# Optimization experiments

Measured on AMD Instinct MI355X. Metric: run time of the kernel, lower is better.

Reference implementation:

```python
import jax, jax.numpy as jnp
import numpy as np

N, E, P, FE = 100000, 400000, 10000, 20000
EMB, L = 300, 5
EPS_BN = 1e-5
EPS_NORM = 1e-12


def setup_inputs() -> dict:
    key = jax.random.key(0)
    ks = iter(jax.random.split(key, 40))

    def nrm(shape, s=0.1):
        return jax.random.normal(next(ks), shape, dtype=jnp.float32) * s

    return {
        "x": jax.random.randint(next(ks), (N, 2), 0, 3),
        "edge_index": jax.random.randint(next(ks), (2, E), 0, N),
        "edge_attr": jax.random.randint(next(ks), (E, 2), 0, 3),
        "frag_batch": jnp.sort(jax.random.randint(next(ks), (N,), 0, P)),
        "frag_edge_index": jax.random.randint(next(ks), (2, FE), 0, P),
        "dangling_edge_attr": jax.random.randint(next(ks), (FE, 2), 0, 3),
        "num_frags": P,
        "atom_emb1": nrm((120, EMB)),
        "atom_emb2": nrm((3, EMB)),
        "gin_e1": nrm((L, 6, EMB)),
        "gin_e2": nrm((L, 3, EMB)),
        "gin_w1": nrm((L, EMB, 2 * EMB), 0.05),
        "gin_b1": jnp.zeros((L, 2 * EMB), jnp.float32),
        "gin_w2": nrm((L, 2 * EMB, EMB), 0.05),
        "gin_b2": jnp.zeros((L, EMB), jnp.float32),
        "bn_g": jnp.ones((L, EMB), jnp.float32),
        "bn_b": jnp.zeros((L, EMB), jnp.float32),
        "proj_w1": nrm((EMB, EMB), 0.05),
        "proj_b1": jnp.zeros((EMB,), jnp.float32),
        "proj_w2": nrm((EMB, EMB), 0.05),
        "proj_b2": jnp.zeros((EMB,), jnp.float32),
        "gcn_w": nrm((EMB, EMB), 0.05),
        "gcn_b": jnp.zeros((EMB,), jnp.float32),
        "gcn_e1": nrm((6, EMB)),
        "gcn_e2": nrm((3, EMB)),
        "cls_w": nrm((EMB, 1), 0.05),
        "cls_b": jnp.zeros((1,), jnp.float32),
    }


def reference(x, edge_index, edge_attr, frag_batch, frag_edge_index,
              dangling_edge_attr, num_frags,
              atom_emb1, atom_emb2, gin_e1, gin_e2, gin_w1, gin_b1, gin_w2,
              gin_b2, bn_g, bn_b, proj_w1, proj_b1, proj_w2, proj_b2,
              gcn_w, gcn_b, gcn_e1, gcn_e2, cls_w, cls_b):
    src, dst = edge_index[0], edge_index[1]
    # --- GNN encoder: 5 GIN layers with edge embeddings + self loops + BN ---
    h = atom_emb1[x[:, 0]] + atom_emb2[x[:, 1]]  # [N, EMB]
    for l in range(L):
        eemb = gin_e1[l][edge_attr[:, 0]] + gin_e2[l][edge_attr[:, 1]]  # [E, EMB]
        agg = jnp.zeros_like(h).at[dst].add(h[src] + eemb)
        # self loops carry bond type 4, direction 0 (pretrain-gnns convention)
        agg = agg + h + (gin_e1[l][4] + gin_e2[l][0])
        h2 = jax.nn.relu(agg @ gin_w1[l] + gin_b1[l]) @ gin_w2[l] + gin_b2[l]
        mu = h2.mean(0)
        var = ((h2 - mu) ** 2).mean(0)  # biased var, torch BN training mode
        h2 = (h2 - mu) * jax.lax.rsqrt(var + EPS_BN) * bn_g[l] + bn_b[l]
        h = h2 if l == L - 1 else jax.nn.relu(h2)
    # --- global mean pool over fragments ---
    seg = jax.ops.segment_sum(h, frag_batch, num_segments=num_frags)
    cnt = jax.ops.segment_sum(jnp.ones((h.shape[0],), h.dtype), frag_batch,
                              num_segments=num_frags)
    pooled = seg / jnp.maximum(cnt, 1.0)[:, None]  # [P, EMB]
    # --- projector MLP ---
    out = jax.nn.relu(pooled @ proj_w1 + proj_b1) @ proj_w2 + proj_b2
    f0 = out / jnp.maximum(jnp.linalg.norm(out, axis=1, keepdims=True), EPS_NORM)
    # --- GCN predictor on symmetrized fragment graph (no self loops) ---
    u = jnp.concatenate([frag_edge_index[0], frag_edge_index[1]])
    v = jnp.concatenate([frag_edge_index[1], frag_edge_index[0]])
    ea = jnp.concatenate([dangling_edge_attr, dangling_edge_attr], axis=0)
    xw = out @ gcn_w + gcn_b
    eemb = gcn_e1[ea[:, 0]] + gcn_e2[ea[:, 1]]
    deg = jnp.zeros((num_frags,), xw.dtype).at[u].add(1.0)
    dis = jnp.where(deg > 0, jax.lax.rsqrt(jnp.maximum(deg, 1.0)), 0.0)
    norm = dis[u] * dis[v]  # deg^-1/2 symmetric normalization
    pred = jnp.zeros_like(xw).at[v].add(norm[:, None] * (xw[u] + eemb))
    f1 = pred / jnp.maximum(jnp.linalg.norm(pred, axis=1, keepdims=True), EPS_NORM)
    f2 = jnp.roll(f1, 1, axis=0)
    # --- classifier on elementwise-max features ---
    pos = jnp.maximum(f0, f1) @ cls_w + cls_b
    neg = jnp.maximum(f0, f2) @ cls_w + cls_b
    return jnp.concatenate([pos, neg], axis=0)[:, 0]  # [2*P]
```

## Files before the change

### kernel.cpp

```cpp
#include <hip/hip_runtime.h>
#include <cstdint>
#include <cstddef>

#define EMB 300
#define EMB2 600
#define NLAYER 5
#define SLD 304
#define KP1 320
#define NP1 640
#define NP2 384
#define SCAN_B 256

typedef short bf16x8 __attribute__((ext_vector_type(8)));
typedef float f32x4 __attribute__((ext_vector_type(4)));
typedef unsigned int u32x4 __attribute__((ext_vector_type(4)));
typedef unsigned short ushort_t;
typedef unsigned int uint_t;

static inline int cdiv(int a, int b) { return (a + b - 1) / b; }

__device__ inline ushort_t f2bf(float v) {
    unsigned u = __float_as_uint(v);
    u += 0x7fffu + ((u >> 16) & 1u);
    return (ushort_t)(u >> 16);
}
__device__ inline float bf2f(ushort_t h) { return __uint_as_float(((unsigned)h) << 16); }

__device__ inline uint_t packbf(float v) {
    ushort_t h = f2bf(v);
    ushort_t l = f2bf(v - bf2f(h));
    return (uint_t)h | ((uint_t)l << 16);
}
__device__ inline u32x4 pack4(f32x4 v) {
    u32x4 w;
    #pragma unroll
    for (int j = 0; j < 4; ++j) w[j] = packbf(v[j]);
    return w;
}

__device__ inline f32x4 bnrelu4(f32x4 v, f32x4 s, f32x4 h, bool use_bn) {
    if (!use_bn) return v;
    f32x4 r;
    #pragma unroll
    for (int j = 0; j < 4; ++j) r[j] = fmaxf(fmaf(v[j], s[j], h[j]), 0.f);
    return r;
}

__global__ __launch_bounds__(256) void zero_kernel(float* __restrict__ p, size_t n)
{
    size_t i = (size_t)blockIdx.x * blockDim.x + threadIdx.x;
    size_t stride = (size_t)gridDim.x * blockDim.x;
    for (; i < n; i += stride) p[i] = 0.f;
}
static inline void launch_zero(float* p, size_t n, hipStream_t s)
{
    int g = (int)((n + 255) / 256);
    if (g > 2048) g = 2048;
    zero_kernel<<<g, 256, 0, s>>>(p, n);
}
__global__ __launch_bounds__(256) void izero_kernel(int* __restrict__ p, int n)
{
    int i = blockIdx.x * 256 + threadIdx.x;
    if (i < n) p[i] = 0;
}

__global__ __launch_bounds__(256) void embed_kernel(
    const int* __restrict__ x, const float* __restrict__ a1,
    const float* __restrict__ a2, float* __restrict__ h, int N)
{
    int idx = blockIdx.x * blockDim.x + threadIdx.x;
    if (idx >= N * EMB) return;
    int row = idx / EMB, col = idx % EMB;
    h[(size_t)row * SLD + col] = a1[x[2 * row] * EMB + col] + a2[x[2 * row + 1] * EMB + col];
}

__global__ __launch_bounds__(256) void count_kernel(
    const int* __restrict__ dst, int* __restrict__ cnt, int E)
{
    int e = blockIdx.x * 256 + threadIdx.x;
    if (e < E) atomicAdd(&cnt[dst[e]], 1);
}

__global__ __launch_bounds__(SCAN_B) void scan_block_kernel(
    const int* __restrict__ in, int* __restrict__ out, int* __restrict__ bsum, int n)
{
    __shared__ int s[SCAN_B];
    int t = threadIdx.x, i = blockIdx.x * SCAN_B + t;
    int v = (i < n) ? in[i] : 0;
    s[t] = v; __syncthreads();
    for (int o = 1; o < SCAN_B; o <<= 1) {
        int xv = (t >= o) ? s[t - o] : 0;
        __syncthreads();
        s[t] += xv;
        __syncthreads();
    }
    if (i < n) out[i] = s[t] - v;
    if (t == SCAN_B - 1) bsum[blockIdx.x] = s[t];
}

__global__ __launch_bounds__(512) void scan_partials_kernel(
    const int* __restrict__ bsum, int* __restrict__ bbase, int nb)
{
    __shared__ int s[512];
    int t = threadIdx.x;
    int v = (t < nb) ? bsum[t] : 0;
    s[t] = v; __syncthreads();
    for (int o = 1; o < 512; o <<= 1) {
        int xv = (t >= o) ? s[t - o] : 0;
        __syncthreads();
        s[t] += xv;
        __syncthreads();
    }
    if (t < nb) bbase[t] = s[t] - v;
}

__global__ __launch_bounds__(256) void scan_add_kernel(
    int* __restrict__ off, const int* __restrict__ bbase, int n, int total)
{
    int i = blockIdx.x * 256 + threadIdx.x;
    if (i < n) off[i] += bbase[i / SCAN_B];
    if (i == 0) off[n] = total;
}

__global__ __launch_bounds__(256) void fill_kernel(
    const int* __restrict__ dst, const int* __restrict__ off,
    int* __restrict__ cursor, int* __restrict__ eid, int E)
{
    int e = blockIdx.x * 256 + threadIdx.x;
    if (e >= E) return;
    int d = dst[e];
    int p = atomicAdd(&cursor[d], 1);
    eid[off[d] + p] = e;
}

__global__ __launch_bounds__(256) void poff_kernel(
    const int* __restrict__ fb, int* __restrict__ poff, int N, int P)
{
    int i = blockIdx.x * 256 + threadIdx.x;
    if (i >= N) return;
    int b = fb[i];
    if (i == 0) { for (int q = 0; q <= b; ++q) poff[q] = 0; }
    else { int a = fb[i - 1]; for (int q = a + 1; q <= b; ++q) poff[q] = i; }
    if (i == N - 1) { for (int q = b + 1; q <= P; ++q) poff[q] = N; }
}

__global__ __launch_bounds__(256) void e12all_kernel(
    const float* __restrict__ ge1, const float* __restrict__ ge2,
    float* __restrict__ E12all)
{
    int idx = blockIdx.x * 256 + threadIdx.x;
    if (idx >= NLAYER * 18 * EMB) return;
    int l = idx / (18 * EMB);
    int rem = idx - l * 18 * EMB;
    int cmb = rem / EMB, c = rem - cmb * EMB;
    E12all[idx] = ge1[(size_t)l * 6 * EMB + (cmb / 3) * EMB + c]
                + ge2[(size_t)l * 3 * EMB + (cmb % 3) * EMB + c];
}

__global__ __launch_bounds__(256) void bn_finalize_kernel(
    const float* __restrict__ stats, const float* __restrict__ g,
    const float* __restrict__ b, float* __restrict__ scale,
    float* __restrict__ shift, float invN)
{
    int c = blockIdx.x * 256 + threadIdx.x;
    if (c >= EMB) return;
    float mu = stats[c] * invN;
    float var = fmaf(-mu, mu, stats[EMB + c] * invN);
    float s = rsqrtf(var + 1e-5f) * g[c];
    scale[c] = s;
    shift[c] = fmaf(-mu, s, b[c]);
}

__global__ __launch_bounds__(256) void gin_gather_il(
    const float* __restrict__ hin, const float* __restrict__ scale,
    const float* __restrict__ shift, int use_bn,
    const int* __restrict__ off, const int* __restrict__ eid,
    const int* __restrict__ src, const int* __restrict__ ea,
    const float* __restrict__ E12, uint_t* __restrict__ Yil, int N)
{
    int node = (blockIdx.x * blockDim.x + threadIdx.x) >> 6;
    int lane = threadIdx.x & 63;
    if (node >= N) return;
    const bool tl = lane < 11;
    const int c0 = lane * 4, c1 = 256 + lane * 4;
    f32x4 sc0 = {1,1,1,1}, sh0 = {0,0,0,0}, sc1 = {1,1,1,1}, sh1 = {0,0,0,0};
    if (use_bn) {
        sc0 = *(const f32x4*)(scale + c0); sh0 = *(const f32x4*)(shift + c0);
        if (tl) { sc1 = *(const f32x4*)(scale + c1); sh1 = *(const f32x4*)(shift + c1); }
    }
    const float* selfrow = E12 + 12 * EMB;
    f32x4 a0, a1 = {0,0,0,0};
    {
        const float* hr = hin + (size_t)node * SLD;
        a0 = bnrelu4(*(const f32x4*)(hr + c0), sc0, sh0, use_bn) + *(const f32x4*)(selfrow + c0);
        if (tl) a1 = bnrelu4(*(const f32x4*)(hr + c1), sc1, sh1, use_bn) + *(const f32x4*)(selfrow + c1);
    }
    int j0 = off[node], j1 = off[node + 1];
    int s = 0, cmb = 0;
    if (j0 < j1) { int e = eid[j0]; s = src[e]; cmb = ea[2 * e] * 3 + ea[2 * e + 1]; }
    for (int j = j0; j < j1; ++j) {
        int sn = 0, cn = 0;
        if (j + 1 < j1) {
            int en = eid[j + 1];
            sn = src[en];
            cn = ea[2 * en] * 3 + ea[2 * en + 1];
        }
        const float* hs = hin + (size_t)s * SLD;
        const float* er = E12 + (size_t)cmb * EMB;
        a0 += bnrelu4(*(const f32x4*)(hs + c0), sc0, sh0, use_bn) + *(const f32x4*)(er + c0);
        if (tl) a1 += bnrelu4(*(const f32x4*)(hs + c1), sc1, sh1, use_bn) + *(const f32x4*)(er + c1);
        s = sn; cmb = cn;
    }
    uint_t* pw = Yil + (size_t)node * SLD;
    *(u32x4*)(pw + c0) = pack4(a0);
    if (tl) *(u32x4*)(pw + c1) = pack4(a1);
}

__global__ __launch_bounds__(256) void gemm_il(
    const uint_t* __restrict__ Ail, int lda, int Mvalid, int Kvalid,
    const ushort_t* __restrict__ Bhi, const ushort_t* __restrict__ Blo, int ldb,
    const float* __restrict__ bias, int Kpad, int Nvalid,
    float* __restrict__ Cf, int ldcf,
    uint_t* __restrict__ Cil, int ldcs,
    int relu, int out_il, float* __restrict__ stats)
{
    __shared__ ushort_t As[2][128][40];
    __shared__ ushort_t Bs[2][128][40];
    __shared__ float cred[128][2];
    const int tid = threadIdx.x;
    const int lane = tid & 63, wid = tid >> 6;
    const int wr = wid >> 1, wc = wid & 1;
    const int lr = lane & 15, ko = (lane >> 4) * 8;

    int gx = gridDim.x;
    int nwg = gx * gridDim.y;
    int flat = blockIdx.y * gx + blockIdx.x;
    if (nwg >= 8) {
        int q = nwg >> 3, r = nwg & 7, xc = flat & 7, s = flat >> 3;
        flat = (xc < r ? xc * (q + 1) : r * (q + 1) + (xc - r) * q) + s;
    }
    const int row0 = (flat / gx) * 128, col0 = (flat % gx) * 128;

    const int srow = tid >> 1;
    const int sc = (tid & 1) * 16;

    const bool arow_ok = (row0 + srow) < Mvalid;
    const uint_t* pA = Ail + (size_t)(row0 + srow) * lda + sc;
    const ushort_t* pBhi = Bhi + (size_t)(col0 + srow) * ldb + sc;
    const ushort_t* pBlo = Blo + (size_t)(col0 + srow) * ldb + sc;
    const u32x4 z4 = {0u, 0u, 0u, 0u};

    f32x4 acc[4][4] = {};
    u32x4 LA[4];
    bf16x8 rB0, rB1, rB2, rB3;

    #pragma unroll
    for (int q = 0; q < 4; ++q) {
        int kc = sc + q * 4;
        LA[q] = (arow_ok && kc < Kvalid) ? *(const u32x4*)(pA + q * 4) : z4;
    }
    rB0 = *(const bf16x8*)(pBhi);     rB1 = *(const bf16x8*)(pBhi + 8);
    rB2 = *(const bf16x8*)(pBlo);     rB3 = *(const bf16x8*)(pBlo + 8);

    for (int k0 = 0; k0 < Kpad; k0 += 32) {
        uint_t hw[8], lw[8];
        #pragma unroll
        for (int i = 0; i < 8; ++i) {
            uint_t w0 = LA[(2 * i) >> 2][(2 * i) & 3];
            uint_t w1 = LA[(2 * i + 1) >> 2][(2 * i + 1) & 3];
            hw[i] = (w0 & 0xFFFFu) | (w1 << 16);
            lw[i] = (w0 >> 16) | (w1 & 0xFFFF0000u);
        }
        *(u32x4*)&As[0][srow][sc]     = (u32x4){hw[0], hw[1], hw[2], hw[3]};
        *(u32x4*)&As[0][srow][sc + 8] = (u32x4){hw[4], hw[5], hw[6], hw[7]};
        *(u32x4*)&As[1][srow][sc]     = (u32x4){lw[0], lw[1], lw[2], lw[3]};
        *(u32x4*)&As[1][srow][sc + 8] = (u32x4){lw[4], lw[5], lw[6], lw[7]};
        *(bf16x8*)&Bs[0][srow][sc]     = rB0;
        *(bf16x8*)&Bs[0][srow][sc + 8] = rB1;
        *(bf16x8*)&Bs[1][srow][sc]     = rB2;
        *(bf16x8*)&Bs[1][srow][sc + 8] = rB3;
        __syncthreads();
        if (k0 + 32 < Kpad) {
            int kn = k0 + 32;
            #pragma unroll
            for (int q = 0; q < 4; ++q) {
                int kc = kn + sc + q * 4;
                LA[q] = (arow_ok && kc < Kvalid) ? *(const u32x4*)(pA + kn + q * 4) : z4;
            }
            rB0 = *(const bf16x8*)(pBhi + kn);     rB1 = *(const bf16x8*)(pBhi + kn + 8);
            rB2 = *(const bf16x8*)(pBlo + kn);     rB3 = *(const bf16x8*)(pBlo + kn + 8);
        }
        bf16x8 afh[4], afl[4], bfh[4], bfl[4];
        #pragma unroll
        for (int f = 0; f < 4; ++f) {
            int ar = wr * 64 + f * 16 + lr;
            afh[f] = *(const bf16x8*)&As[0][ar][ko];
            afl[f] = *(const bf16x8*)&As[1][ar][ko];
            int bc = wc * 64 + f * 16 + lr;
            bfh[f] = *(const bf16x8*)&Bs[0][bc][ko];
            bfl[f] = *(const bf16x8*)&Bs[1][bc][ko];
        }
        #pragma unroll
        for (int f = 0; f < 4; ++f)
            #pragma unroll
            for (int g = 0; g < 4; ++g) {
                acc[f][g] = __builtin_amdgcn_mfma_f32_16x16x32_bf16(afh[f], bfh[g], acc[f][g], 0, 0, 0);
                acc[f][g] = __builtin_amdgcn_mfma_f32_16x16x32_bf16(afh[f], bfl[g], acc[f][g], 0, 0, 0);
                acc[f][g] = __builtin_amdgcn_mfma_f32_16x16x32_bf16(afl[f], bfh[g], acc[f][g], 0, 0, 0);
            }
        __syncthreads();
    }

    float ts[4] = {0.f, 0.f, 0.f, 0.f}, ts2[4] = {0.f, 0.f, 0.f, 0.f};
    #pragma unroll
    for (int f = 0; f < 4; ++f) {
        int grb = row0 + wr * 64 + f * 16 + (lane >> 4) * 4;
        #pragma unroll
        for (int g = 0; g < 4; ++g) {
            int gc = col0 + wc * 64 + g * 16 + lr;
            float bv = (gc < Nvalid) ? bias[gc] : 0.f;
            #pragma unroll
            for (int j = 0; j < 4; ++j) {
                int gr = grb + j;
                float v = acc[f][g][j] + bv;
                if (relu) v = fmaxf(v, 0.f);
                if (out_il) {
                    float vp = (gc < Nvalid) ? v : 0.f;
                    Cil[(size_t)gr * ldcs + gc] = packbf(vp);
                } else if (gr < Mvalid && gc < Nvalid) {
                    Cf[(size_t)gr * ldcf + gc] = v;
                    if (stats) {
                        ts[g] += v;
                        ts2[g] = fmaf(v, v, ts2[g]);
                    }
                }
            }
        }
    }
    if (stats && !out_il) {
        ((float*)cred)[tid] = 0.f;
        __syncthreads();
        #pragma unroll
        for (int g = 0; g < 4; ++g) {
            int cidx = wc * 64 + g * 16 + lr;
            atomicAdd(&cred[cidx][0], ts[g]);
            atomicAdd(&cred[cidx][1], ts2[g]);
        }
        __syncthreads();
        if (tid < 128) {
            int gc = col0 + tid;
            if (gc < Nvalid) {
                atomicAdd(&stats[gc], cred[tid][0]);
                atomicAdd(&stats[EMB + gc], cred[tid][1]);
            }
        }
    }
}

#define TS 64
#define BKK 16
__global__ __launch_bounds__(256) void gemm_bias_act(
    const float* __restrict__ A, const float* __restrict__ W,
    const float* __restrict__ bias, float* __restrict__ C,
    int M, int K, int Nc, int relu_flag)
{
    __shared__ float Asm[BKK][TS + 4];
    __shared__ float Bsm[BKK][TS + 4];
    const int tid = threadIdx.x;
    const int tx = tid & 15, ty = tid >> 4;
    const int row0 = blockIdx.y * TS, col0 = blockIdx.x * TS;
    const int lka = tid & 15, lra = tid >> 4;
    const int lnb = tid & 63, lkb = tid >> 6;
    float acc[4][4] = {};
    for (int k0 = 0; k0 < K; k0 += BKK) {
        #pragma unroll
        for (int i = 0; i < 4; ++i) {
            int rr = lra + 16 * i;
            int gr = row0 + rr, gk = k0 + lka;
            Asm[lka][rr] = (gr < M && gk < K) ? A[(size_t)gr * K + gk] : 0.f;
        }
        #pragma unroll
        for (int i = 0; i < 4; ++i) {
            int kk = lkb + 4 * i;
            int gk = k0 + kk, gn = col0 + lnb;
            Bsm[kk][lnb] = (gk < K && gn < Nc) ? W[(size_t)gk * Nc + gn] : 0.f;
        }
        __syncthreads();
        #pragma unroll
        for (int kk = 0; kk < BKK; ++kk) {
            float a[4], b[4];
            #pragma unroll
            for (int i = 0; i < 4; ++i) a[i] = Asm[kk][ty * 4 + i];
            #pragma unroll
            for (int j = 0; j < 4; ++j) b[j] = Bsm[kk][tx * 4 + j];
            #pragma unroll
            for (int i = 0; i < 4; ++i)
                #pragma unroll
                for (int j = 0; j < 4; ++j)
                    acc[i][j] = fmaf(a[i], b[j], acc[i][j]);
        }
        __syncthreads();
    }
    #pragma unroll
    for (int i = 0; i < 4; ++i) {
        int gr = row0 + ty * 4 + i;
        if (gr >= M) continue;
        #pragma unroll
        for (int j = 0; j < 4; ++j) {
            int gn = col0 + tx * 4 + j;
            if (gn >= Nc) continue;
            float v = acc[i][j] + bias[gn];
            if (relu_flag) v = fmaxf(v, 0.f);
            C[(size_t)gr * Nc + gn] = v;
        }
    }
}

__global__ __launch_bounds__(256) void wsplit_kernel(
    const float* __restrict__ W, int K, int Nc,
    ushort_t* __restrict__ hi, ushort_t* __restrict__ lo, int Kpad, int Npad)
{
    int idx = blockIdx.x * 256 + threadIdx.x;
    if (idx >= Npad * Kpad) return;
    int n = idx / Kpad, k = idx - n * Kpad;
    float v = (n < Nc && k < K) ? W[(size_t)k * Nc + n] : 0.f;
    ushort_t h = f2bf(v);
    hi[idx] = h;
    lo[idx] = f2bf(v - bf2f(h));
}

__global__ __launch_bounds__(256) void pool_gather_kernel(
    const float* __restrict__ hin, const float* __restrict__ scale,
    const float* __restrict__ shift, const int* __restrict__ poff,
    float* __restrict__ pooled, int P)
{
    int p = (blockIdx.x * blockDim.x + threadIdx.x) >> 6;
    int lane = threadIdx.x & 63;
    if (p >= P) return;
    const bool tl = lane < 11;
    const int c0 = lane * 4, c1 = 256 + lane * 4;
    int r0 = poff[p], r1 = poff[p + 1];
    f32x4 s0 = {0,0,0,0}, s1 = {0,0,0,0};
    for (int r = r0; r < r1; ++r) {
        const float* hr = hin + (size_t)r * SLD;
        s0 += *(const f32x4*)(hr + c0);
        if (tl) s1 += *(const f32x4*)(hr + c1);
    }
    float cntf = (float)(r1 - r0);
    float inv = 1.f / fmaxf(cntf, 1.f);
    f32x4 sc0 = *(const f32x4*)(scale + c0), sh0 = *(const f32x4*)(shift + c0);
    f32x4 o0;
    #pragma unroll
    for (int j = 0; j < 4; ++j) o0[j] = fmaf(s0[j], sc0[j], cntf * sh0[j]) * inv;
    float* pr = pooled + (size_t)p * EMB;
    *(f32x4*)(pr + c0) = o0;
    if (tl) {
        f32x4 sc1 = *(const f32x4*)(scale + c1), sh1 = *(const f32x4*)(shift + c1);
        f32x4 o1;
        #pragma unroll
        for (int j = 0; j < 4; ++j) o1[j] = fmaf(s1[j], sc1[j], cntf * sh1[j]) * inv;
        *(f32x4*)(pr + c1) = o1;
    }
}

__global__ __launch_bounds__(256) void normalize_rows_kernel(
    const float* __restrict__ X, float* __restrict__ Y, int M)
{
    int wv = (blockIdx.x * blockDim.x + threadIdx.x) >> 6;
    int lane = threadIdx.x & 63;
    if (wv >= M) return;
    const float* x = X + (size_t)wv * EMB;
    float ss = 0.f;
    for (int c = lane; c < EMB; c += 64) { float v = x[c]; ss = fmaf(v, v, ss); }
    #pragma unroll
    for (int o = 32; o > 0; o >>= 1) ss += __shfl_xor(ss, o, 64);
    float inv = 1.f / fmaxf(sqrtf(ss), 1e-12f);
    float* y = Y + (size_t)wv * EMB;
    for (int c = lane; c < EMB; c += 64) y[c] = x[c] * inv;
}

__global__ __launch_bounds__(256) void deg_kernel(
    const int* __restrict__ fei, float* __restrict__ deg, int FE)
{
    int i = blockIdx.x * blockDim.x + threadIdx.x;
    if (i < 2 * FE) atomicAdd(&deg[fei[i]], 1.f);
}

__global__ __launch_bounds__(256) void gcn_scatter_kernel(
    const float* __restrict__ xw, const int* __restrict__ fei,
    const int* __restrict__ dea, const float* __restrict__ e1,
    const float* __restrict__ e2, const float* __restrict__ deg,
    float* __restrict__ pred, int FE)
{
    int i = (blockIdx.x * blockDim.x + threadIdx.x) >> 6;
    int lane = threadIdx.x & 63;
    if (i >= 2 * FE) return;
    int u = fei[i];
    int v = (i < FE) ? fei[i + FE] : fei[i - FE];
    int er = (i < FE) ? i : i - FE;
    int a0 = dea[2 * er], a1 = dea[2 * er + 1];
    float du = deg[u], dv = deg[v];
    float su = du > 0.f ? rsqrtf(fmaxf(du, 1.f)) : 0.f;
    float sv = dv > 0.f ? rsqrtf(fmaxf(dv, 1.f)) : 0.f;
    float nr = su * sv;
    const float* xu = xw + (size_t)u * EMB;
    const float* t1 = e1 + (size_t)a0 * EMB;
    const float* t2 = e2 + (size_t)a1 * EMB;
    float* pv = pred + (size_t)v * EMB;
    for (int c = lane; c < EMB; c += 64)
        atomicAdd(&pv[c], nr * (xu[c] + t1[c] + t2[c]));
}

__global__ __launch_bounds__(256) void classifier_kernel(
    const float* __restrict__ f0, const float* __restrict__ f1,
    const float* __restrict__ w, const float* __restrict__ b,
    float* __restrict__ out, int P)
{
    int q = (blockIdx.x * blockDim.x + threadIdx.x) >> 6;
    int lane = threadIdx.x & 63;
    if (q >= 2 * P) return;
    int i = (q < P) ? q : q - P;
    int j = (q < P) ? i : (i == 0 ? P - 1 : i - 1);
    const float* a = f0 + (size_t)i * EMB;
    const float* c = f1 + (size_t)j * EMB;
    float s = 0.f;
    for (int k = lane; k < EMB; k += 64) s = fmaf(fmaxf(a[k], c[k]), w[k], s);
    #pragma unroll
    for (int o = 32; o > 0; o >>= 1) s += __shfl_xor(s, o, 64);
    if (lane == 0) out[q] = s + b[0];
}

extern "C" void kernel_launch(void* const* d_in, const int* in_sizes, int n_in,
                              void* d_out, int out_size, void* d_ws, size_t ws_size,
                              hipStream_t stream)
{
    const int*   x     = (const int*)d_in[0];
    const int*   ei    = (const int*)d_in[1];
    const int*   ea    = (const int*)d_in[2];
    const int*   fb    = (const int*)d_in[3];
    const int*   fei   = (const int*)d_in[4];
    const int*   dea   = (const int*)d_in[5];
    const float* atom1 = (const float*)d_in[7];
    const float* atom2 = (const float*)d_in[8];
    const float* ge1   = (const float*)d_in[9];
    const float* ge2   = (const float*)d_in[10];
    const float* w1    = (const float*)d_in[11];
    const float* b1    = (const float*)d_in[12];
    const float* w2    = (const float*)d_in[13];
    const float* b2    = (const float*)d_in[14];
    const float* bng   = (const float*)d_in[15];
    const float* bnb   = (const float*)d_in[16];
    const float* pw1   = (const float*)d_in[17];
    const float* pb1   = (const float*)d_in[18];
    const float* pw2   = (const float*)d_in[19];
    const float* pb2   = (const float*)d_in[20];
    const float* gw    = (const float*)d_in[21];
    const float* gb    = (const float*)d_in[22];
    const float* gcne1 = (const float*)d_in[23];
    const float* gcne2 = (const float*)d_in[24];
    const float* clw   = (const float*)d_in[25];
    const float* clb   = (const float*)d_in[26];
    (void)n_in; (void)ws_size;

    const int N  = in_sizes[0] / 2;
    const int E  = in_sizes[1] / 2;
    const int FE = in_sizes[4] / 2;
    const int P  = out_size / 2;
    const int Mfull = cdiv(N, 128) * 128;
    float* outF = (float*)d_out;

    char* wp = (char*)d_ws;
    auto carve = [&](size_t bytes) -> char* {
        char* r = wp;
        wp += (bytes + 255) & ~(size_t)255;
        return r;
    };
    const size_t bufElems = (size_t)Mfull * SLD;
    char* bufA = carve(bufElems * 4);
    char* bufB = carve(bufElems * 4);
    float* statsAll = (float*)carve((size_t)NLAYER * 2 * EMB * 4);
    float* scaleAll = (float*)carve((size_t)NLAYER * EMB * 4);
    float* shiftAll = (float*)carve((size_t)NLAYER * EMB * 4);
    float* E12all   = (float*)carve((size_t)NLAYER * 18 * EMB * 4);
    float* deg      = (float*)carve((size_t)P * 4);
    int* poff    = (int*)carve((size_t)(P + 1) * 4);
    int* cnt_i   = (int*)carve((size_t)N * 4);
    int* csr_off = (int*)carve((size_t)(N + 1) * 4);
    int* cursor  = (int*)carve((size_t)N * 4);
    int* csr_eid = (int*)carve((size_t)E * 4);
    int* bsum    = (int*)carve(512 * 4);
    int* bbase   = (int*)carve(512 * 4);
    ushort_t* w1t_hi[NLAYER]; ushort_t* w1t_lo[NLAYER];
    ushort_t* w2t_hi[NLAYER]; ushort_t* w2t_lo[NLAYER];
    for (int l = 0; l < NLAYER; ++l) {
        w1t_hi[l] = (ushort_t*)carve((size_t)NP1 * KP1 * 2);
        w1t_lo[l] = (ushort_t*)carve((size_t)NP1 * KP1 * 2);
        w2t_hi[l] = (ushort_t*)carve((size_t)NP2 * NP1 * 2);
        w2t_lo[l] = (ushort_t*)carve((size_t)NP2 * NP1 * 2);
    }

    int chCap = (int)((bufElems * 4) / ((size_t)NP1 * 4));
    chCap &= ~127;
    int nChunks = cdiv(Mfull, chCap);
    int CH = cdiv(Mfull / 128, nChunks) * 128;

    const int gElemsN = cdiv(N * EMB, 256);
    const int NB = cdiv(N, SCAN_B);

    izero_kernel<<<cdiv(N, 256), 256, 0, stream>>>(cnt_i, N);
    count_kernel<<<cdiv(E, 256), 256, 0, stream>>>(ei + E, cnt_i, E);
    scan_block_kernel<<<NB, SCAN_B, 0, stream>>>(cnt_i, csr_off, bsum, N);
    scan_partials_kernel<<<1, 512, 0, stream>>>(bsum, bbase, NB);
    scan_add_kernel<<<cdiv(N, 256), 256, 0, stream>>>(csr_off, bbase, N, E);
    izero_kernel<<<cdiv(N, 256), 256, 0, stream>>>(cursor, N);
    fill_kernel<<<cdiv(E, 256), 256, 0, stream>>>(ei + E, csr_off, cursor, csr_eid, E);
    poff_kernel<<<cdiv(N, 256), 256, 0, stream>>>(fb, poff, N, P);
    e12all_kernel<<<cdiv(NLAYER * 18 * EMB, 256), 256, 0, stream>>>(ge1, ge2, E12all);
    for (int l = 0; l < NLAYER; ++l) {
        wsplit_kernel<<<cdiv(NP1 * KP1, 256), 256, 0, stream>>>(
            w1 + (size_t)l * EMB * EMB2, EMB, EMB2, w1t_hi[l], w1t_lo[l], KP1, NP1);
        wsplit_kernel<<<cdiv(NP2 * NP1, 256), 256, 0, stream>>>(
            w2 + (size_t)l * EMB2 * EMB, EMB2, EMB, w2t_hi[l], w2t_lo[l], NP1, NP2);
    }
    launch_zero(statsAll, (size_t)NLAYER * 2 * EMB, stream);

    embed_kernel<<<gElemsN, 256, 0, stream>>>(x, atom1, atom2, (float*)bufA, N);

    char* ping = bufA;
    char* pong = bufB;
    for (int l = 0; l < NLAYER; ++l) {
        gin_gather_il<<<cdiv(N, 4), 256, 0, stream>>>(
            (const float*)ping,
            scaleAll + (size_t)(l > 0 ? l - 1 : 0) * EMB,
            shiftAll + (size_t)(l > 0 ? l - 1 : 0) * EMB, (l > 0) ? 1 : 0,
            csr_off, csr_eid, ei, ea, E12all + (size_t)l * 18 * EMB,
            (uint_t*)pong, N);
        uint_t* til = (uint_t*)ping;
        for (int c0 = 0; c0 < N; c0 += CH) {
            int rows = min(CH, N - c0);
            int Mt = cdiv(rows, 128);
            gemm_il<<<dim3(NP1 / 128, Mt), 256, 0, stream>>>(
                (const uint_t*)pong + (size_t)c0 * SLD, SLD, rows, EMB,
                w1t_hi[l], w1t_lo[l], KP1,
                b1 + (size_t)l * EMB2, KP1, EMB2,
                nullptr, 0, til, NP1, 1, 1, nullptr);
            gemm_il<<<dim3(NP2 / 128, Mt), 256, 0, stream>>>(
                til, NP1, rows, NP1,
                w2t_hi[l], w2t_lo[l], NP1,
                b2 + (size_t)l * EMB, NP1, EMB,
                (float*)pong + (size_t)c0 * SLD, SLD, nullptr, 0, 0, 0,
                statsAll + (size_t)l * 2 * EMB);
        }
        bn_finalize_kernel<<<cdiv(EMB, 256), 256, 0, stream>>>(
            statsAll + (size_t)l * 2 * EMB, bng + (size_t)l * EMB, bnb + (size_t)l * EMB,
            scaleAll + (size_t)l * EMB, shiftAll + (size_t)l * EMB, 1.f / (float)N);
        char* tmp = ping; ping = pong; pong = tmp;
    }

    float* Af     = (float*)pong;
    float* pooled = Af + 0 * (size_t)P * EMB;
    float* tmpP   = Af + 1 * (size_t)P * EMB;
    float* outp   = Af + 2 * (size_t)P * EMB;
    float* f0     = Af + 3 * (size_t)P * EMB;
    float* xw     = Af + 4 * (size_t)P * EMB;
    float* pred   = Af + 5 * (size_t)P * EMB;
    float* f1     = Af + 6 * (size_t)P * EMB;

    pool_gather_kernel<<<cdiv(P, 4), 256, 0, stream>>>(
        (const float*)ping, scaleAll + (size_t)(NLAYER - 1) * EMB,
        shiftAll + (size_t)(NLAYER - 1) * EMB, poff, pooled, P);

    {
        dim3 g1(cdiv(EMB, TS), cdiv(P, TS));
        gemm_bias_act<<<g1, 256, 0, stream>>>(pooled, pw1, pb1, tmpP, P, EMB, EMB, 1);
        gemm_bias_act<<<g1, 256, 0, stream>>>(tmpP, pw2, pb2, outp, P, EMB, EMB, 0);
        normalize_rows_kernel<<<cdiv(P, 4), 256, 0, stream>>>(outp, f0, P);
    }

    {
        dim3 g1(cdiv(EMB, TS), cdiv(P, TS));
        gemm_bias_act<<<g1, 256, 0, stream>>>(outp, gw, gb, xw, P, EMB, EMB, 0);
        launch_zero(deg, (size_t)P, stream);
        launch_zero(pred, (size_t)P * EMB, stream);
        deg_kernel<<<cdiv(2 * FE, 256), 256, 0, stream>>>(fei, deg, FE);
        gcn_scatter_kernel<<<cdiv(2 * FE, 4), 256, 0, stream>>>(
            xw, fei, dea, gcne1, gcne2, deg, pred, FE);
        normalize_rows_kernel<<<cdiv(P, 4), 256, 0, stream>>>(pred, f1, P);
    }

    classifier_kernel<<<cdiv(2 * P, 4), 256, 0, stream>>>(f0, f1, clw, clb, outF, P);
}
```

Before: 3.405 ms.

## Route projector and GCN GEMMs through split-bf16 MFMA kernel, nontemporal gather stores

Replaces the scalar FP32 tiled GEMM used for the projector MLP and GCN weight transform with the existing split-bf16 MFMA gemm_il kernel. Pooling now writes interleaved bf16 hi/lo output, and the GEMM gains an output mode that writes both fp32 and interleaved forms so chained GEMMs can consume it directly. The weights are pre-split at startup. GIN gather outputs switch to nontemporal stores. This adds three wsplit launches and padded buffers, and the split-bf16 path may differ slightly in numerics from full FP32.

```diff
diff --git a/kernel.cpp b/kernel.cpp
--- a/kernel.cpp
+++ b/kernel.cpp
@@ -212,8 +212,8 @@
         s = sn; cmb = cn;
     }
     uint_t* pw = Yil + (size_t)node * SLD;
-    *(u32x4*)(pw + c0) = pack4(a0);
-    if (tl) *(u32x4*)(pw + c1) = pack4(a1);
+    __builtin_nontemporal_store(pack4(a0), (u32x4*)(pw + c0));
+    if (tl) __builtin_nontemporal_store(pack4(a1), (u32x4*)(pw + c1));
 }
 
 __global__ __launch_bounds__(256) void gemm_il(
@@ -222,7 +222,7 @@
     const float* __restrict__ bias, int Kpad, int Nvalid,
     float* __restrict__ Cf, int ldcf,
     uint_t* __restrict__ Cil, int ldcs,
-    int relu, int out_il, float* __restrict__ stats)
+    int relu, int out_mode, float* __restrict__ stats)
 {
     __shared__ ushort_t As[2][128][40];
     __shared__ ushort_t Bs[2][128][40];
@@ -324,20 +324,23 @@
                 int gr = grb + j;
                 float v = acc[f][g][j] + bv;
                 if (relu) v = fmaxf(v, 0.f);
-                if (out_il) {
+                if (out_mode != 1) {
+                    if (gr < Mvalid && gc < Nvalid) {
+                        Cf[(size_t)gr * ldcf + gc] = v;
+                        if (stats) {
+                            ts[g] += v;
+                            ts2[g] = fmaf(v, v, ts2[g]);
+                        }
+                    }
+                }
+                if (out_mode >= 1) {
                     float vp = (gc < Nvalid) ? v : 0.f;
                     Cil[(size_t)gr * ldcs + gc] = packbf(vp);
-                } else if (gr < Mvalid && gc < Nvalid) {
-                    Cf[(size_t)gr * ldcf + gc] = v;
-                    if (stats) {
-                        ts[g] += v;
-                        ts2[g] = fmaf(v, v, ts2[g]);
-                    }
                 }
             }
         }
     }
-    if (stats && !out_il) {
+    if (stats && out_mode != 1) {
         ((float*)cred)[tid] = 0.f;
         __syncthreads();
         #pragma unroll
@@ -353,65 +356,6 @@
                 atomicAdd(&stats[gc], cred[tid][0]);
                 atomicAdd(&stats[EMB + gc], cred[tid][1]);
             }
-        }
-    }
-}
-
-#define TS 64
-#define BKK 16
-__global__ __launch_bounds__(256) void gemm_bias_act(
-    const float* __restrict__ A, const float* __restrict__ W,
-    const float* __restrict__ bias, float* __restrict__ C,
-    int M, int K, int Nc, int relu_flag)
-{
-    __shared__ float Asm[BKK][TS + 4];
-    __shared__ float Bsm[BKK][TS + 4];
-    const int tid = threadIdx.x;
-    const int tx = tid & 15, ty = tid >> 4;
-    const int row0 = blockIdx.y * TS, col0 = blockIdx.x * TS;
-    const int lka = tid & 15, lra = tid >> 4;
-    const int lnb = tid & 63, lkb = tid >> 6;
-    float acc[4][4] = {};
-    for (int k0 = 0; k0 < K; k0 += BKK) {
-        #pragma unroll
-        for (int i = 0; i < 4; ++i) {
-            int rr = lra + 16 * i;
-            int gr = row0 + rr, gk = k0 + lka;
-            Asm[lka][rr] = (gr < M && gk < K) ? A[(size_t)gr * K + gk] : 0.f;
-        }
-        #pragma unroll
-        for (int i = 0; i < 4; ++i) {
-            int kk = lkb + 4 * i;
-            int gk = k0 + kk, gn = col0 + lnb;
-            Bsm[kk][lnb] = (gk < K && gn < Nc) ? W[(size_t)gk * Nc + gn] : 0.f;
-        }
-        __syncthreads();
-        #pragma unroll
-        for (int kk = 0; kk < BKK; ++kk) {
-            float a[4], b[4];
-            #pragma unroll
-            for (int i = 0; i < 4; ++i) a[i] = Asm[kk][ty * 4 + i];
-            #pragma unroll
-            for (int j = 0; j < 4; ++j) b[j] = Bsm[kk][tx * 4 + j];
-            #pragma unroll
-            for (int i = 0; i < 4; ++i)
-                #pragma unroll
-                for (int j = 0; j < 4; ++j)
-                    acc[i][j] = fmaf(a[i], b[j], acc[i][j]);
-        }
-        __syncthreads();
-    }
-    #pragma unroll
-    for (int i = 0; i < 4; ++i) {
-        int gr = row0 + ty * 4 + i;
-        if (gr >= M) continue;
-        #pragma unroll
-        for (int j = 0; j < 4; ++j) {
-            int gn = col0 + tx * 4 + j;
-            if (gn >= Nc) continue;
-            float v = acc[i][j] + bias[gn];
-            if (relu_flag) v = fmaxf(v, 0.f);
-            C[(size_t)gr * Nc + gn] = v;
         }
     }
 }
@@ -429,10 +373,10 @@
     lo[idx] = f2bf(v - bf2f(h));
 }
 
-__global__ __launch_bounds__(256) void pool_gather_kernel(
+__global__ __launch_bounds__(256) void pool_gather_il(
     const float* __restrict__ hin, const float* __restrict__ scale,
     const float* __restrict__ shift, const int* __restrict__ poff,
-    float* __restrict__ pooled, int P)
+    uint_t* __restrict__ pooledIl, int P)
 {
     int p = (blockIdx.x * blockDim.x + threadIdx.x) >> 6;
     int lane = threadIdx.x & 63;
@@ -452,14 +396,14 @@
     f32x4 o0;
     #pragma unroll
     for (int j = 0; j < 4; ++j) o0[j] = fmaf(s0[j], sc0[j], cntf * sh0[j]) * inv;
-    float* pr = pooled + (size_t)p * EMB;
-    *(f32x4*)(pr + c0) = o0;
+    uint_t* pr = pooledIl + (size_t)p * KP1;
+    *(u32x4*)(pr + c0) = pack4(o0);
     if (tl) {
         f32x4 sc1 = *(const f32x4*)(scale + c1), sh1 = *(const f32x4*)(shift + c1);
         f32x4 o1;
         #pragma unroll
         for (int j = 0; j < 4; ++j) o1[j] = fmaf(s1[j], sc1[j], cntf * sh1[j]) * inv;
-        *(f32x4*)(pr + c1) = o1;
+        *(u32x4*)(pr + c1) = pack4(o1);
     }
 }
 
@@ -567,6 +511,7 @@
     const int FE = in_sizes[4] / 2;
     const int P  = out_size / 2;
     const int Mfull = cdiv(N, 128) * 128;
+    const int PM = cdiv(P, 128) * 128;
     float* outF = (float*)d_out;
 
     char* wp = (char*)d_ws;
@@ -598,6 +543,12 @@
         w2t_hi[l] = (ushort_t*)carve((size_t)NP2 * NP1 * 2);
         w2t_lo[l] = (ushort_t*)carve((size_t)NP2 * NP1 * 2);
     }
+    ushort_t* pw1t_hi = (ushort_t*)carve((size_t)NP2 * KP1 * 2);
+    ushort_t* pw1t_lo = (ushort_t*)carve((size_t)NP2 * KP1 * 2);
+    ushort_t* pw2t_hi = (ushort_t*)carve((size_t)NP2 * NP2 * 2);
+    ushort_t* pw2t_lo = (ushort_t*)carve((size_t)NP2 * NP2 * 2);
+    ushort_t* gwt_hi  = (ushort_t*)carve((size_t)NP2 * NP2 * 2);
+    ushort_t* gwt_lo  = (ushort_t*)carve((size_t)NP2 * NP2 * 2);
 
     int chCap = (int)((bufElems * 4) / ((size_t)NP1 * 4));
     chCap &= ~127;
@@ -622,6 +573,9 @@
         wsplit_kernel<<<cdiv(NP2 * NP1, 256), 256, 0, stream>>>(
             w2 + (size_t)l * EMB2 * EMB, EMB2, EMB, w2t_hi[l], w2t_lo[l], NP1, NP2);
     }
+    wsplit_kernel<<<cdiv(NP2 * KP1, 256), 256, 0, stream>>>(pw1, EMB, EMB, pw1t_hi, pw1t_lo, KP1, NP2);
+    wsplit_kernel<<<cdiv(NP2 * NP2, 256), 256, 0, stream>>>(pw2, EMB, EMB, pw2t_hi, pw2t_lo, NP2, NP2);
+    wsplit_kernel<<<cdiv(NP2 * NP2, 256), 256, 0, stream>>>(gw,  EMB, EMB, gwt_hi,  gwt_lo,  NP2, NP2);
     launch_zero(statsAll, (size_t)NLAYER * 2 * EMB, stream);
 
     embed_kernel<<<gElemsN, 256, 0, stream>>>(x, atom1, atom2, (float*)bufA, N);
@@ -657,36 +611,43 @@
         char* tmp = ping; ping = pong; pong = tmp;
     }
 
-    float* Af     = (float*)pong;
-    float* pooled = Af + 0 * (size_t)P * EMB;
-    float* tmpP   = Af + 1 * (size_t)P * EMB;
-    float* outp   = Af + 2 * (size_t)P * EMB;
-    float* f0     = Af + 3 * (size_t)P * EMB;
-    float* xw     = Af + 4 * (size_t)P * EMB;
-    float* pred   = Af + 5 * (size_t)P * EMB;
-    float* f1     = Af + 6 * (size_t)P * EMB;
-
-    pool_gather_kernel<<<cdiv(P, 4), 256, 0, stream>>>(
+    char* ap = pong;
+    auto acv = [&](size_t bytes) -> char* {
+        char* r = ap;
+        ap += (bytes + 255) & ~(size_t)255;
+        return r;
+    };
+    float*  outp     = (float*)acv((size_t)P * EMB * 4);
+    float*  f0       = (float*)acv((size_t)P * EMB * 4);
+    float*  xw       = (float*)acv((size_t)P * EMB * 4);
+    float*  pred     = (float*)acv((size_t)P * EMB * 4);
+    float*  f1       = (float*)acv((size_t)P * EMB * 4);
+    uint_t* pooledIl = (uint_t*)acv((size_t)PM * KP1 * 4);
+    uint_t* tmpIl    = (uint_t*)acv((size_t)PM * NP2 * 4);
+    uint_t* outIl    = (uint_t*)acv((size_t)PM * NP2 * 4);
+
+    pool_gather_il<<<cdiv(P, 4), 256, 0, stream>>>(
         (const float*)ping, scaleAll + (size_t)(NLAYER - 1) * EMB,
-        shiftAll + (size_t)(NLAYER - 1) * EMB, poff, pooled, P);
-
-    {
-        dim3 g1(cdiv(EMB, TS), cdiv(P, TS));
-        gemm_bias_act<<<g1, 256, 0, stream>>>(pooled, pw1, pb1, tmpP, P, EMB, EMB, 1);
-        gemm_bias_act<<<g1, 256, 0, stream>>>(tmpP, pw2, pb2, outp, P, EMB, EMB, 0);
-        normalize_rows_kernel<<<cdiv(P, 4), 256, 0, stream>>>(outp, f0, P);
-    }
-
-    {
-        dim3 g1(cdiv(EMB, TS), cdiv(P, TS));
-        gemm_bias_act<<<g1, 256, 0, stream>>>(outp, gw, gb, xw, P, EMB, EMB, 0);
-        launch_zero(deg, (size_t)P, stream);
-        launch_zero(pred, (size_t)P * EMB, stream);
-        deg_kernel<<<cdiv(2 * FE, 256), 256, 0, stream>>>(fei, deg, FE);
-        gcn_scatter_kernel<<<cdiv(2 * FE, 4), 256, 0, stream>>>(
-            xw, fei, dea, gcne1, gcne2, deg, pred, FE);
-        normalize_rows_kernel<<<cdiv(P, 4), 256, 0, stream>>>(pred, f1, P);
-    }
+        shiftAll + (size_t)(NLAYER - 1) * EMB, poff, pooledIl, P);
+
+    const int MtP = PM / 128;
+    gemm_il<<<dim3(NP2 / 128, MtP), 256, 0, stream>>>(
+        pooledIl, KP1, P, EMB, pw1t_hi, pw1t_lo, KP1,
+        pb1, KP1, EMB, nullptr, 0, tmpIl, NP2, 1, 1, nullptr);
+    gemm_il<<<dim3(NP2 / 128, MtP), 256, 0, stream>>>(
+        tmpIl, NP2, P, NP2, pw2t_hi, pw2t_lo, NP2,
+        pb2, NP2, EMB, outp, EMB, outIl, NP2, 0, 2, nullptr);
+    normalize_rows_kernel<<<cdiv(P, 4), 256, 0, stream>>>(outp, f0, P);
+
+    gemm_il<<<dim3(NP2 / 128, MtP), 256, 0, stream>>>(
+        outIl, NP2, P, NP2, gwt_hi, gwt_lo, NP2,
+        gb, NP2, EMB, xw, EMB, nullptr, 0, 0, 0, nullptr);
+    launch_zero(deg, (size_t)P, stream);
+    launch_zero(pred, (size_t)P * EMB, stream);
+    deg_kernel<<<cdiv(2 * FE, 256), 256, 0, stream>>>(fei, deg, FE);
+    gcn_scatter_kernel<<<cdiv(2 * FE, 4), 256, 0, stream>>>(
+        xw, fei, dea, gcne1, gcne2, deg, pred, FE);
+    normalize_rows_kernel<<<cdiv(P, 4), 256, 0, stream>>>(pred, f1, P);
 
     classifier_kernel<<<cdiv(2 * P, 4), 256, 0, stream>>>(f0, f1, clw, clb, outF, P);
 }
```

After: 3.393 ms. No clear change (-0.4%).
